# Kernel tuning notes

Measured on AMD Instinct MI355X. Metric: run time of the kernel, lower is better.

## Reference

```python
import jax, jax.numpy as jnp
import numpy as np

DEGREE = 3          # hardcoded in BSplineLoss
NUM_SAMPLES = 20    # hardcoded in BSplineLoss
B, N = 65536, 64


def setup_inputs() -> dict:
    key = jax.random.key(0)
    k1, k2 = jax.random.split(key)

    def make_seq(kk):
        ka, kb = jax.random.split(kk)
        # strictly increasing positive knots (valid B-spline knot vector)
        incr = jax.random.uniform(ka, (B, N), minval=0.1, maxval=1.0)
        knots = jnp.cumsum(incr, axis=1)
        coeffs = jax.random.normal(kb, (B, N, 2))
        return jnp.concatenate([knots[..., None], coeffs], axis=-1)  # [B,N,3]

    pred_seq = make_seq(k1)
    true_seq = make_seq(k2)
    true_masks = jnp.ones((B, N), dtype=jnp.int32)  # full-length splines
    return {"pred_seq": pred_seq, "true_seq": true_seq, "true_masks": true_masks}


def _deboor_sample(coeffs, knots):
    """Vectorized De Boor evaluation.
    coeffs: [B,n,2], knots: [B,n] -> samples [B,NUM_SAMPLES,2].
    Mirrors BSpline._interpolate with weights==1."""
    b, n, d = coeffs.shape
    dt = coeffs.dtype
    # prepend degree+1 zeros: full knot vector [B, n+degree+1]
    kf = jnp.concatenate([jnp.zeros((b, DEGREE + 1), dt), knots], axis=1)
    low = kf[:, DEGREE]          # knots[domain[0]]
    high = kf[:, n]              # knots[domain[1]] (domain[1] = n+degree - degree = n)
    t = jnp.linspace(0.0, 1.0, NUM_SAMPLES, dtype=dt)[None] * (high - low)[:, None] + low[:, None]  # [B,T]
    inner = kf[:, DEGREE:n]      # knots[domain[0]:domain[1]]
    s = jax.vmap(lambda a, v: jnp.searchsorted(a, v, side='right'))(inner, t) + DEGREE - 1  # [B,T]

    # homogeneous control points (weights = 1)
    v = jnp.concatenate([coeffs, jnp.ones((b, n, 1), dt)], axis=-1)  # [B,n,3]

    karr = jnp.arange(DEGREE + 1)               # local window index 0..degree
    idx = s[..., None] - DEGREE + karr          # [B,T,degree+1] global control indices
    bidx = jnp.arange(b)[:, None, None]
    p = v[bidx, idx]                            # [B,T,degree+1,3] local De Boor window

    for l in range(1, DEGREE + 1):  # l = degree+1 level does no work in the original
        ki = kf[bidx, idx]                       # knots[i]
        kj = kf[bidx, idx + DEGREE + 1 - l]      # knots[i+degree+1-l]
        denom = kj - ki
        safe = jnp.where(denom != 0, denom, jnp.ones((), dt))
        alpha = jnp.where(denom != 0, (t[..., None] - ki) / safe, jnp.zeros((), dt))  # [B,T,4]
        shifted = jnp.concatenate([p[:, :, :1], p[:, :, :-1]], axis=2)  # p[k-1]
        cand = (1.0 - alpha)[..., None] * shifted + alpha[..., None] * p
        p = jnp.where((karr >= l)[None, None, :, None], cand, p)

    return p[:, :, DEGREE, :d] / p[:, :, DEGREE, d:]  # [B,T,2]


def reference(pred_seq, true_seq, true_masks):
    pred_knots, pred_coeffs = pred_seq[:, :, 0], pred_seq[:, :, 1:3]
    true_knots, true_coeffs = true_seq[:, :, 0], true_seq[:, :, 1:3]
    # masks are all ones -> ragged selection is identity
    sampled_true = _deboor_sample(true_coeffs, true_knots)
    sampled_pred = _deboor_sample(pred_coeffs, pred_knots)
    mask = jnp.ones(sampled_true.shape[:2], sampled_true.dtype)  # [B,20]
    mse = (sampled_pred - sampled_true) ** 2
    return (mse * mask[..., None]).sum() / mask.sum()
```

## Files before the change

### kernel.cpp

```cpp
#include <hip/hip_runtime.h>

#define DEG 3
#define NSAMP 20
#define BROWS 65536
#define NKNOT 64
#define ROWS_PER_BLOCK 4
#define NBLOCKS (BROWS / ROWS_PER_BLOCK)

__global__ __launch_bounds__(256) void bspline_loss_main(
    const float* __restrict__ pred, const float* __restrict__ tru,
    float* __restrict__ partials)
{
    __shared__ float lds[ROWS_PER_BLOCK][2][192];
    __shared__ float wsum[ROWS_PER_BLOCK];

    const int tid  = threadIdx.x;
    const int wave = tid >> 6;
    const int lane = tid & 63;
    const int row  = blockIdx.x * ROWS_PER_BLOCK + wave;

    if (lane < 48) {
        const float4 p4 = ((const float4*)(pred + (size_t)row * 192))[lane];
        const float4 t4 = ((const float4*)(tru  + (size_t)row * 192))[lane];
        ((float4*)lds[wave][0])[lane] = p4;
        ((float4*)lds[wave][1])[lane] = t4;
    }
    __syncthreads();

    float rx = 0.f, ry = 0.f;
    if (lane < 40) {
        const int sel = (lane >= 20) ? 1 : 0;
        const int s   = sel ? lane - 20 : lane;
        const float* d = lds[wave][sel];

        const float high = d[3 * 60];
        const float t = ((float)s * (1.0f / 19.0f)) * high;

        int lo = 0, hi = 60;
        while (lo < hi) {
            int mid = (lo + hi) >> 1;
            if (d[3 * mid] <= t) lo = mid + 1; else hi = mid;
        }
        const int cnt = lo;

        float px[4], py[4], pw[4];
        #pragma unroll
        for (int k = 0; k < 4; ++k) {
            px[k] = d[3 * (cnt + k) + 1];
            py[k] = d[3 * (cnt + k) + 2];
            pw[k] = 1.0f;
        }
        #pragma unroll
        for (int l = 1; l <= DEG; ++l) {
            #pragma unroll
            for (int k = DEG; k >= l; --k) {
                const int i0 = cnt + k;
                const int i1 = cnt + k + (DEG + 1 - l);
                const float ki = (i0 < 4) ? 0.f : d[3 * (i0 - 4)];
                const float kj = (i1 < 4) ? 0.f : d[3 * (i1 - 4)];
                const float denom = kj - ki;
                const float alpha = (denom != 0.f) ? (t - ki) / denom : 0.f;
                const float b0 = 1.0f - alpha;
                px[k] = b0 * px[k - 1] + alpha * px[k];
                py[k] = b0 * py[k - 1] + alpha * py[k];
                pw[k] = b0 * pw[k - 1] + alpha * pw[k];
            }
        }
        rx = px[DEG] / pw[DEG];
        ry = py[DEG] / pw[DEG];
    }

    const float ox = __shfl(rx, lane + 20, 64);
    const float oy = __shfl(ry, lane + 20, 64);
    float acc = 0.f;
    if (lane < 20) {
        const float dx = rx - ox, dy = ry - oy;
        acc = dx * dx + dy * dy;
    }
    #pragma unroll
    for (int off = 32; off >= 1; off >>= 1)
        acc += __shfl_down(acc, off, 64);
    if (lane == 0) wsum[wave] = acc;
    __syncthreads();
    if (tid == 0)
        partials[blockIdx.x] = wsum[0] + wsum[1] + wsum[2] + wsum[3];
}

__global__ __launch_bounds__(256) void bspline_loss_reduce(
    const float* __restrict__ partials, float* __restrict__ out)
{
    const int tid = threadIdx.x;
    double acc = 0.0;
    const float4* p4 = (const float4*)partials;
    #pragma unroll 4
    for (int i = tid; i < NBLOCKS / 4; i += 256) {
        const float4 v = p4[i];
        acc += (double)v.x + (double)v.y + (double)v.z + (double)v.w;
    }
    #pragma unroll
    for (int off = 32; off >= 1; off >>= 1)
        acc += __shfl_down(acc, off, 64);
    __shared__ double ws[4];
    if ((tid & 63) == 0) ws[tid >> 6] = acc;
    __syncthreads();
    if (tid == 0) {
        const double tot = ws[0] + ws[1] + ws[2] + ws[3];
        out[0] = (float)(tot / (double)((long long)BROWS * NSAMP));
    }
}

extern "C" void kernel_launch(void* const* d_in, const int* in_sizes, int n_in,
                              void* d_out, int out_size, void* d_ws, size_t ws_size,
                              hipStream_t stream) {
    const float* pred = (const float*)d_in[0];
    const float* tru  = (const float*)d_in[1];
    float* out      = (float*)d_out;
    float* partials = (float*)d_ws;

    bspline_loss_main<<<NBLOCKS, 256, 0, stream>>>(pred, tru, partials);
    bspline_loss_reduce<<<1, 256, 0, stream>>>(partials, out);
}
```

Measured before the change: 132.8 us.

## Pack 8 rows per 320-thread block so every lane evaluates a sample

Restructures the main kernel so 320 threads handle 8 rows (40 samples per row across 8 rows), where before 40 of 64 lanes per wave did work. The pred/true pairing moves from wave shuffles to LDS arrays with an extra barrier, because a row's samples can now cross wave boundaries. The cooperative load uses a padded segment stride, and a redundant bounds check on the right knot index is dropped. The intent is to use lanes fully and halve the block count, at the cost of an extra LDS round trip and barrier.

After: 133.0 us, median of 2. No clear change (+0.2%).

```diff
diff --git a/kernel.cpp b/kernel.cpp
--- a/kernel.cpp
+++ b/kernel.cpp
@@ -4,86 +4,93 @@
 #define NSAMP 20
 #define BROWS 65536
 #define NKNOT 64
-#define ROWS_PER_BLOCK 4
+#define ROWS_PER_BLOCK 8
+#define THREADS 320
 #define NBLOCKS (BROWS / ROWS_PER_BLOCK)
+#define SEG 196
 
-__global__ __launch_bounds__(256) void bspline_loss_main(
+__global__ __launch_bounds__(THREADS) void bspline_loss_main(
     const float* __restrict__ pred, const float* __restrict__ tru,
     float* __restrict__ partials)
 {
-    __shared__ float lds[ROWS_PER_BLOCK][2][192];
-    __shared__ float wsum[ROWS_PER_BLOCK];
+    __shared__ float lds[ROWS_PER_BLOCK * 2 * SEG];
+    __shared__ float sx[ROWS_PER_BLOCK * 40];
+    __shared__ float sy[ROWS_PER_BLOCK * 40];
+    __shared__ float wsum[THREADS / 64];
 
-    const int tid  = threadIdx.x;
-    const int wave = tid >> 6;
-    const int lane = tid & 63;
-    const int row  = blockIdx.x * ROWS_PER_BLOCK + wave;
+    const int tid = threadIdx.x;
 
-    if (lane < 48) {
-        const float4 p4 = ((const float4*)(pred + (size_t)row * 192))[lane];
-        const float4 t4 = ((const float4*)(tru  + (size_t)row * 192))[lane];
-        ((float4*)lds[wave][0])[lane] = p4;
-        ((float4*)lds[wave][1])[lane] = t4;
+    {
+        const float4* p4 = (const float4*)(pred + (size_t)blockIdx.x * (ROWS_PER_BLOCK * 192));
+        const float4* t4 = (const float4*)(tru  + (size_t)blockIdx.x * (ROWS_PER_BLOCK * 192));
+        for (int i = tid; i < ROWS_PER_BLOCK * 48; i += THREADS) {
+            const int r = i / 48;
+            const int j = i - r * 48;
+            ((float4*)(lds + (r * 2 + 0) * SEG))[j] = p4[i];
+            ((float4*)(lds + (r * 2 + 1) * SEG))[j] = t4[i];
+        }
     }
     __syncthreads();
 
-    float rx = 0.f, ry = 0.f;
-    if (lane < 40) {
-        const int sel = (lane >= 20) ? 1 : 0;
-        const int s   = sel ? lane - 20 : lane;
-        const float* d = lds[wave][sel];
+    const int rloc = tid / 40;
+    const int rem  = tid - rloc * 40;
+    const int sel  = (rem >= 20) ? 1 : 0;
+    const int s    = rem - sel * 20;
+    const float* d = lds + (rloc * 2 + sel) * SEG;
 
-        const float high = d[3 * 60];
-        const float t = ((float)s * (1.0f / 19.0f)) * high;
+    const float high = d[3 * 60];
+    const float t = ((float)s * (1.0f / 19.0f)) * high;
 
-        int lo = 0, hi = 60;
-        while (lo < hi) {
-            int mid = (lo + hi) >> 1;
-            if (d[3 * mid] <= t) lo = mid + 1; else hi = mid;
+    int lo = 0, hi = 60;
+    while (lo < hi) {
+        int mid = (lo + hi) >> 1;
+        if (d[3 * mid] <= t) lo = mid + 1; else hi = mid;
+    }
+    const int cnt = lo;
+
+    float px[4], py[4], pw[4];
+    #pragma unroll
+    for (int k = 0; k < 4; ++k) {
+        px[k] = d[3 * (cnt + k) + 1];
+        py[k] = d[3 * (cnt + k) + 2];
+        pw[k] = 1.0f;
+    }
+    #pragma unroll
+    for (int l = 1; l <= DEG; ++l) {
+        #pragma unroll
+        for (int k = DEG; k >= l; --k) {
+            const int i0 = cnt + k;
+            const int i1 = cnt + k + (DEG + 1 - l);
+            const float ki = (i0 < 4) ? 0.f : d[3 * (i0 - 4)];
+            const float kj = d[3 * (i1 - 4)];
+            const float denom = kj - ki;
+            const float alpha = (denom != 0.f) ? (t - ki) / denom : 0.f;
+            const float b0 = 1.0f - alpha;
+            px[k] = b0 * px[k - 1] + alpha * px[k];
+            py[k] = b0 * py[k - 1] + alpha * py[k];
+            pw[k] = b0 * pw[k - 1] + alpha * pw[k];
         }
-        const int cnt = lo;
+    }
+    const float rx = px[DEG] / pw[DEG];
+    const float ry = py[DEG] / pw[DEG];
 
-        float px[4], py[4], pw[4];
-        #pragma unroll
-        for (int k = 0; k < 4; ++k) {
-            px[k] = d[3 * (cnt + k) + 1];
-            py[k] = d[3 * (cnt + k) + 2];
-            pw[k] = 1.0f;
-        }
-        #pragma unroll
-        for (int l = 1; l <= DEG; ++l) {
-            #pragma unroll
-            for (int k = DEG; k >= l; --k) {
-                const int i0 = cnt + k;
-                const int i1 = cnt + k + (DEG + 1 - l);
-                const float ki = (i0 < 4) ? 0.f : d[3 * (i0 - 4)];
-                const float kj = (i1 < 4) ? 0.f : d[3 * (i1 - 4)];
-                const float denom = kj - ki;
-                const float alpha = (denom != 0.f) ? (t - ki) / denom : 0.f;
-                const float b0 = 1.0f - alpha;
-                px[k] = b0 * px[k - 1] + alpha * px[k];
-                py[k] = b0 * py[k - 1] + alpha * py[k];
-                pw[k] = b0 * pw[k - 1] + alpha * pw[k];
-            }
-        }
-        rx = px[DEG] / pw[DEG];
-        ry = py[DEG] / pw[DEG];
-    }
+    sx[tid] = rx;
+    sy[tid] = ry;
+    __syncthreads();
 
-    const float ox = __shfl(rx, lane + 20, 64);
-    const float oy = __shfl(ry, lane + 20, 64);
     float acc = 0.f;
-    if (lane < 20) {
-        const float dx = rx - ox, dy = ry - oy;
+    if (!sel) {
+        const float dx = rx - sx[tid + 20];
+        const float dy = ry - sy[tid + 20];
         acc = dx * dx + dy * dy;
     }
     #pragma unroll
     for (int off = 32; off >= 1; off >>= 1)
         acc += __shfl_down(acc, off, 64);
-    if (lane == 0) wsum[wave] = acc;
+    if ((tid & 63) == 0) wsum[tid >> 6] = acc;
     __syncthreads();
     if (tid == 0)
-        partials[blockIdx.x] = wsum[0] + wsum[1] + wsum[2] + wsum[3];
+        partials[blockIdx.x] = wsum[0] + wsum[1] + wsum[2] + wsum[3] + wsum[4];
 }
 
 __global__ __launch_bounds__(256) void bspline_loss_reduce(
@@ -117,6 +124,6 @@
     float* out      = (float*)d_out;
     float* partials = (float*)d_ws;
 
-    bspline_loss_main<<<NBLOCKS, 256, 0, stream>>>(pred, tru, partials);
+    bspline_loss_main<<<NBLOCKS, THREADS, 0, stream>>>(pred, tru, partials);
     bspline_loss_reduce<<<1, 256, 0, stream>>>(partials, out);
 }
```
